# Optimization experiments

Hardware: AMD Instinct MI355X
Metric: run time of the kernel (lower is better)

## Reference

```python
import jax, jax.numpy as jnp
import numpy as np

B, S, D, H = 4, 1024, 1024, 16
HD = D // H  # per-head dim = 64
NEG = -10000000000.0


def setup_inputs() -> dict:
    key = jax.random.key(0)
    ks = jax.random.split(key, 12)
    q = jax.random.normal(ks[0], (B, S, D), jnp.float32)
    k = jax.random.normal(ks[1], (B, S, D), jnp.float32)
    v = jax.random.normal(ks[2], (B, S, D), jnp.float32)
    mask = jax.random.randint(ks[3], (B, S, S), 0, 2).astype(jnp.int32)
    sc = 1.0 / np.sqrt(D)
    Wq = jax.random.normal(ks[4], (H, D, HD), jnp.float32) * sc
    bq = jnp.zeros((H, HD), jnp.float32)
    Wk = jax.random.normal(ks[5], (H, D, HD), jnp.float32) * sc
    bk = jnp.zeros((H, HD), jnp.float32)
    Wv = jax.random.normal(ks[6], (H, D, HD), jnp.float32) * sc
    bv = jnp.zeros((H, HD), jnp.float32)
    Wo = jax.random.normal(ks[7], (D, D), jnp.float32) * sc
    bo = jnp.zeros((D,), jnp.float32)
    return {"query": q, "key": k, "value": v, "attention_mask": mask,
            "Wq": Wq, "bq": bq, "Wk": Wk, "bk": bk, "Wv": Wv, "bv": bv,
            "Wo": Wo, "bo": bo}


def reference(query, key, value, attention_mask, Wq, bq, Wk, bk, Wv, bv, Wo, bo):
    # batched per-head projections: [B,S,D] x [H,D,E] -> [B,H,S,E]
    q = jnp.einsum('bsd,hde->bhse', query, Wq) + bq[None, :, None, :]
    k = jnp.einsum('bsd,hde->bhse', key, Wk) + bk[None, :, None, :]
    v = jnp.einsum('bsd,hde->bhse', value, Wv) + bv[None, :, None, :]
    # NOTE: scale uses key_dim (model_size = full D), faithful to source
    score = jnp.einsum('bhse,bhte->bhst', q, k) / jnp.sqrt(jnp.float32(D))
    m = attention_mask.astype(jnp.float32)[:, None, :, :]  # [B,1,S,S]
    score = score + (1.0 - m) * NEG
    attn = jax.nn.softmax(score, axis=-1) * m  # double masking
    heads = jnp.einsum('bhst,bhte->bhse', attn, v)  # [B,H,S,E]
    # concat heads along feature dim (head order preserved)
    heads = heads.transpose(0, 2, 1, 3).reshape(B, S, D)
    return heads @ Wo + bo
```

## Files before the change

kernel.cpp:

```cpp
#include <hip/hip_runtime.h>

#define B_ 4
#define S_ 1024
#define D_ 1024
#define H_ 16
#define E_ 64
#define BS_ (B_*S_)
#define BHSE_ (B_*H_*S_*E_)

typedef __attribute__((ext_vector_type(8))) short bf16x8;
typedef __attribute__((ext_vector_type(4))) float f32x4;
typedef __attribute__((ext_vector_type(4))) unsigned int u32x4;

__device__ __forceinline__ unsigned short f2bf(float f) {
    unsigned int x = __float_as_uint(f);
    x = (x + 0x7FFFu + ((x >> 16) & 1u)) >> 16;
    return (unsigned short)x;
}
__device__ __forceinline__ float bf2f(unsigned short u) {
    return __uint_as_float(((unsigned int)u) << 16);
}
__device__ __forceinline__ float ldin(const void* p, size_t i, int isb) {
    return isb ? bf2f(((const unsigned short*)p)[i]) : ((const float*)p)[i];
}

__device__ __forceinline__ unsigned int cvtpk(float lo, float hi) {
    unsigned int r;
    asm("v_cvt_pk_bf16_f32 %0, %1, %2" : "=v"(r) : "v"(lo), "v"(hi));
    return r;
}
__device__ __forceinline__ unsigned int bperm(int srclane4, unsigned int v) {
    return (unsigned int)__builtin_amdgcn_ds_bpermute(srclane4, (int)v);
}
__device__ __forceinline__ bf16x8 u4bf(u32x4 w) {
    union { u32x4 u; bf16x8 h; } c; c.u = w; return c.h;
}

#if __has_builtin(__builtin_amdgcn_exp2f)
#define EXP2(x) __builtin_amdgcn_exp2f(x)
#else
#define EXP2(x) __expf((x) * 0.6931471805599453f)
#endif

__device__ __forceinline__ void gl2lds16(const void* g, void* l) {
    __builtin_amdgcn_global_load_lds(
        (const __attribute__((address_space(1))) void*)g,
        (__attribute__((address_space(3))) void*)l, 16, 0, 0);
}

__global__ void detect_dtype(const unsigned int* q, int* flag) {
    __shared__ int cnt;
    if (threadIdx.x == 0) cnt = 0;
    __syncthreads();
    unsigned int w = q[threadIdx.x];
    unsigned int lo = w & 0xFFFFu;
    unsigned int e = (lo >> 7) & 0xFFu;
    int ok = (lo == 0u) || (e >= 100u && e <= 145u);
    atomicAdd(&cnt, ok);
    __syncthreads();
    if (threadIdx.x == 0) flag[0] = (cnt >= 240) ? 1 : 0;
}

__global__ __launch_bounds__(256) void conv_w2(
        const void* Wq, const void* Wk, const void* Wv, const void* Wo,
        const void* bq_, const void* bk_, const void* bv_, const void* bo_,
        unsigned short* WT, float* biases, const int* flag) {
    __shared__ unsigned short Tt[64][72];
    const int isb = flag[0];
    const int z = blockIdx.z, t = threadIdx.x;
    const void* src = (z == 0) ? Wq : (z == 1) ? Wk : (z == 2) ? Wv : Wo;
    const int r0 = blockIdx.y * 64;
    const int c0 = blockIdx.x;
    {
        int dl = t >> 2, qc = t & 3;
        size_t base;
        if (z < 3) base = (size_t)c0 * 65536 + (size_t)(r0 + dl) * 64 + qc * 16;
        else       base = (size_t)(r0 + dl) * 1024 + (size_t)c0 * 64 + qc * 16;
        if (isb) {
            const unsigned short* s = (const unsigned short*)src + base;
            bf16x8 a0 = *(const bf16x8*)s, a1 = *(const bf16x8*)(s + 8);
#pragma unroll
            for (int j = 0; j < 8; j++) {
                Tt[qc * 16 + j][dl] = (unsigned short)a0[j];
                Tt[qc * 16 + 8 + j][dl] = (unsigned short)a1[j];
            }
        } else {
            const float* s = (const float*)src + base;
#pragma unroll
            for (int j = 0; j < 16; j++) Tt[qc * 16 + j][dl] = f2bf(s[j]);
        }
    }
    __syncthreads();
    {
        int el = t >> 2, qc = t & 3;
        size_t dst = (size_t)z * D_ * D_ + (size_t)(c0 * 64 + el) * D_ + r0 + qc * 16;
        *(bf16x8*)&WT[dst]     = *(const bf16x8*)&Tt[el][qc * 16];
        *(bf16x8*)&WT[dst + 8] = *(const bf16x8*)&Tt[el][qc * 16 + 8];
    }
    if (z == 3 && blockIdx.y == 0 && blockIdx.x < 4) {
        const void* bs = (blockIdx.x == 0) ? bq_ : (blockIdx.x == 1) ? bk_
                       : (blockIdx.x == 2) ? bv_ : bo_;
#pragma unroll
        for (int j = 0; j < 4; j++) {
            int i = t * 4 + j;
            biases[blockIdx.x * 1024 + i] = ldin(bs, i, isb);
        }
    }
}

__global__ void maskpack(const int* mask, unsigned long long* packT) {
    int W = blockIdx.x * 4 + (threadIdx.x >> 6);
    int lane = threadIdx.x & 63;
    int b = W >> 14, rem = W & 16383, s = rem >> 4, kt = rem & 15;
    int mv = mask[((size_t)b * 1024 + s) * 1024 + kt * 64 + lane];
    unsigned long long bits = __ballot(mv != 0);
    if (lane == 0) packT[((size_t)b * 16 + kt) * 1024 + s] = bits;
}

__global__ __launch_bounds__(256) void conv_a(
        const float* q, const float* k, const float* v,
        unsigned short* dst, const int* flag) {
    if (flag[0]) return;
    const int z = blockIdx.x >> 11;
    const float* s = (z == 0) ? q : (z == 1) ? k : v;
    const size_t i = ((size_t)(blockIdx.x & 2047) * 256 + threadIdx.x) * 8;
    f32x4 a0 = *(const f32x4*)(s + i);
    f32x4 a1 = *(const f32x4*)(s + i + 4);
    bf16x8 o;
#pragma unroll
    for (int j = 0; j < 4; j++) {
        o[j]     = (short)f2bf(a0[j]);
        o[4 + j] = (short)f2bf(a1[j]);
    }
    *(bf16x8*)&dst[(size_t)z * ((size_t)BS_ * D_) + i] = o;
}

template<int BM, int BN, int MODE, int MINW>
__global__ __launch_bounds__(256, MINW) void gemm_k(
        const void* A0, const void* A1, const void* A2, const unsigned short* Aconv,
        const unsigned short* BtB, const float* biasB, void* dstB, const int* flag) {
    constexpr int TOT16 = (BM + BN) * 32;
    constexpr int CALLS = TOT16 / 512;
    constexpr int CPW = CALLS / 4;
    constexpr int MT = BM / 32;
    constexpr int NT = BN / 32;
    __shared__ unsigned short buf[2][TOT16];

    const int t = threadIdx.x, lane = t & 63, w = t >> 6;
    const int lm = lane & 15, q4 = lane >> 4;
    const int wm = w >> 1, wn = w & 1;
    const int lr = lane >> 2;
    const int ls = lane & 3;
    const int lg = ls ^ ((lr >> 1) & 3);
    const int fl = flag[0];

    const unsigned short* Abf;
    const unsigned short* Bt;
    const float* bias;
    int z = 0, m0, n0, phase;
    if (MODE == 0) {
        int bid = blockIdx.x + (blockIdx.y << 5) + (blockIdx.z << 9);
        int xcd = bid & 7, idx = bid >> 3;
        z = idx >> 6;
        int r = idx & 63;
        int mt = (xcd << 2) + (r & 3);
        int nt = r >> 2;
        m0 = mt * BM; n0 = nt * BN;
        phase = (nt * 13 + z * 5) & 31;
        const void* Ain = (z == 0) ? A0 : (z == 1 ? A1 : A2);
        Abf = fl ? (const unsigned short*)Ain
                 : Aconv + (size_t)z * ((size_t)BS_ * D_);
        Bt = BtB + (size_t)z * D_ * D_;
        bias = biasB + z * 1024;
    } else {
        Abf = (const unsigned short*)A0;
        Bt = BtB; bias = biasB;
        m0 = blockIdx.x * BM; n0 = blockIdx.y * BN;
        phase = (blockIdx.x * 7 + blockIdx.y * 13) & 31;
    }

    auto stage = [&](int kk, int bi) {
#pragma unroll
        for (int i = 0; i < CPW; ++i) {
            int c = w * CPW + i;
            int row = c * 16 + lr;
            const unsigned short* g;
            if (row < BM)
                g = Abf + (size_t)(m0 + row) * D_ + kk + lg * 8;
            else
                g = Bt + (size_t)(n0 + row - BM) * D_ + kk + lg * 8;
            gl2lds16(g, &buf[bi][c * 512]);
        }
    };

    f32x4 acc[MT][NT];
#pragma unroll
    for (int i = 0; i < MT; i++)
#pragma unroll
        for (int j = 0; j < NT; j++) acc[i][j] = (f32x4){0.f, 0.f, 0.f, 0.f};

    stage((phase & 31) * 32, 0);
    for (int it = 0; it < D_ / 32; ++it) {
        const int bi = it & 1;
        __syncthreads();
        if (it < D_ / 32 - 1) stage(((it + 1 + phase) & 31) * 32, bi ^ 1);

        const unsigned short* As = buf[bi];
        const unsigned short* Bs = buf[bi] + BM * 32;
        bf16x8 af[MT], bv[NT];
#pragma unroll
        for (int mt = 0; mt < MT; mt++) {
            int row = wm * (BM / 2) + mt * 16 + lm;
            af[mt] = *(const bf16x8*)&As[row * 32 + (q4 ^ ((row >> 1) & 3)) * 8];
        }
#pragma unroll
        for (int nt = 0; nt < NT; nt++) {
            int row = wn * (BN / 2) + nt * 16 + lm;
            bv[nt] = *(const bf16x8*)&Bs[row * 32 + (q4 ^ ((row >> 1) & 3)) * 8];
        }
#pragma unroll
        for (int mt = 0; mt < MT; mt++)
#pragma unroll
            for (int nt = 0; nt < NT; nt++)
                acc[mt][nt] = __builtin_amdgcn_mfma_f32_16x16x32_bf16(
                    af[mt], bv[nt], acc[mt][nt], 0, 0, 0);
    }

#pragma unroll
    for (int mt = 0; mt < MT; mt++)
#pragma unroll
        for (int nt = 0; nt < NT; nt++) {
            int N = n0 + wn * (BN / 2) + nt * 16 + lm;
            int Mb = m0 + wm * (BM / 2) + mt * 16 + q4 * 4;
            if (MODE == 0 && z == 2) {
                int bb = Mb >> 10, sb = Mb & 1023, hh = N >> 6, e = N & 63;
                unsigned long long hv = 0;
#pragma unroll
                for (int r = 0; r < 4; r++)
                    hv |= (unsigned long long)f2bf(acc[mt][nt][r] + bias[N]) << (16 * r);
                unsigned short* d16 = (unsigned short*)dstB + (size_t)2 * BHSE_;
                *(unsigned long long*)&d16[(((size_t)(bb * H_ + hh) * E_ + e) << 10) + sb] = hv;
            } else {
#pragma unroll
                for (int r = 0; r < 4; r++) {
                    int M = Mb + r;
                    float v = acc[mt][nt][r] + bias[N];
                    if (MODE == 0) {
                        int bb = M >> 10, s = M & 1023, hh = N >> 6, e = N & 63;
                        unsigned short* d16 = (unsigned short*)dstB + (size_t)z * BHSE_;
                        d16[((size_t)(bb * H_ + hh) * S_ + s) * E_ + e] = f2bf(v);
                    } else {
                        size_t idx = (size_t)M * D_ + N;
                        if (fl) ((unsigned short*)dstB)[idx] = f2bf(v);
                        else    ((float*)dstB)[idx] = v;
                    }
                }
            }
        }
}

__global__ __launch_bounds__(256, 5) void attn64(
        const unsigned short* Qp, const unsigned short* Kp, const unsigned short* VpT,
        const unsigned long long* packT, unsigned short* heads) {
    __shared__ unsigned short KT[2][4096];
    __shared__ unsigned short VT[2][4096];

    const int qt = blockIdx.x, h = blockIdx.y, b = blockIdx.z;
    const int t = threadIdx.x, w = t >> 6, lane = t & 63, lm = lane & 15, q4 = lane >> 4;
    const size_t bh = ((size_t)b * H_ + h) * S_ * E_;
    const unsigned short* Qb = Qp + bh;
    const unsigned short* Kb = Kp + bh;
    const unsigned short* Vb = VpT + bh;
    const int q0 = qt * 64 + w * 16;

    const int l3 = lane >> 3, l7 = lane & 7;
    const int kLaneOff = l3 * 64 + (l7 ^ l3) * 8;
    const int vLaneOff = l3 * 1024 + (l7 ^ l3) * 8;

    const int sw = lm & 7;
    const int c0 = (q4 ^ sw) * 8, c1 = ((q4 ^ 4) ^ sw) * 8;

    const int srcA4 = ((lane & 15) | ((lane & 16) << 1)) << 2;
    const int srcB4 = srcA4 + 64;
    const bool selHi = (lane & 32) != 0;

    bf16x8 bq0 = *(const bf16x8*)&Qb[(size_t)(q0 + lm) * E_ + q4 * 8];
    bf16x8 bq1 = *(const bf16x8*)&Qb[(size_t)(q0 + lm) * E_ + 32 + q4 * 8];

    f32x4 oacc[4];
#pragma unroll
    for (int i = 0; i < 4; i++) oacc[i] = (f32x4){0.f, 0.f, 0.f, 0.f};
    float mrun = -3.0e38f, lrun = 0.f;
    const float scale2 = 0.03125f * 1.4426950408889634f;

#define STAGE(ktile, bufi)                                                    \
    {                                                                         \
        int k0s = (ktile) * 64;                                               \
        _Pragma("unroll")                                                     \
        for (int i_ = 0; i_ < 4; ++i_) {                                      \
            int c_ = w * 4 + i_;                                              \
            if (c_ < 8) {                                                     \
                gl2lds16(Kb + (size_t)k0s * 64 + c_ * 512 + kLaneOff,         \
                         &KT[bufi][c_ * 512]);                                \
            } else {                                                          \
                int cc_ = c_ - 8;                                             \
                gl2lds16(Vb + (size_t)cc_ * 8192 + k0s + vLaneOff,            \
                         &VT[bufi][cc_ * 512]);                               \
            }                                                                 \
        }                                                                     \
    }

    STAGE(0, 0)

    for (int kt = 0; kt < S_ / 64; ++kt) {
        const int bufi = kt & 1;
        __syncthreads();
        if (kt < 15) STAGE(kt + 1, bufi ^ 1)

        unsigned long long mk = packT[((size_t)b * 16 + kt) * 1024 + q0 + lm];

        f32x4 st[4];
#pragma unroll
        for (int jt = 0; jt < 4; ++jt) {
            const unsigned short* kr = &KT[bufi][(jt * 16 + lm) * 64];
            bf16x8 ka0 = *(const bf16x8*)&kr[c0];
            bf16x8 ka1 = *(const bf16x8*)&kr[c1];
            f32x4 zz = (f32x4){0.f, 0.f, 0.f, 0.f};
            zz = __builtin_amdgcn_mfma_f32_16x16x32_bf16(ka0, bq0, zz, 0, 0, 0);
            zz = __builtin_amdgcn_mfma_f32_16x16x32_bf16(ka1, bq1, zz, 0, 0, 0);
            st[jt] = zz;
        }

        float tmx = -3.0e38f;
#pragma unroll
        for (int jt = 0; jt < 4; ++jt)
#pragma unroll
            for (int r = 0; r < 4; r++) tmx = fmaxf(tmx, st[jt][r]);
        tmx = fmaxf(tmx, __shfl_xor(tmx, 16, 64));
        tmx = fmaxf(tmx, __shfl_xor(tmx, 32, 64));
        float pmax = tmx * scale2;

        if (!__all(pmax - mrun <= 8.f)) {
            float mnew = fmaxf(mrun, pmax);
            float alpha = EXP2(mrun - mnew);
            lrun *= alpha;
#pragma unroll
            for (int nt = 0; nt < 4; nt++) oacc[nt] = oacc[nt] * alpha;
            mrun = mnew;
        }
        const float mneg = -mrun;

        unsigned int mn = (unsigned int)(mk >> (q4 * 4));
        unsigned int mh = (unsigned int)(mk >> (q4 * 4 + 32));

        float ssum = 0.f;
        unsigned int cl[8];
#pragma unroll
        for (int jt = 0; jt < 4; ++jt) {
            unsigned int mm = (jt & 2) ? mh : mn;
            const int sh = (jt & 1) * 16;
            float p0 = EXP2(fmaf(st[jt][0], scale2, mneg));
            float p1 = EXP2(fmaf(st[jt][1], scale2, mneg));
            float p2 = EXP2(fmaf(st[jt][2], scale2, mneg));
            float p3 = EXP2(fmaf(st[jt][3], scale2, mneg));
            p0 = (mm & (1u << (sh + 0))) ? p0 : 0.f;
            p1 = (mm & (1u << (sh + 1))) ? p1 : 0.f;
            p2 = (mm & (1u << (sh + 2))) ? p2 : 0.f;
            p3 = (mm & (1u << (sh + 3))) ? p3 : 0.f;
            ssum += (p0 + p1) + (p2 + p3);
            cl[jt * 2]     = cvtpk(p0, p1);
            cl[jt * 2 + 1] = cvtpk(p2, p3);
        }
        ssum += __shfl_xor(ssum, 16, 64);
        ssum += __shfl_xor(ssum, 32, 64);
        lrun += ssum;

        u32x4 w0, w1;
        {
            unsigned int aA0 = bperm(srcA4, cl[0]), aA2 = bperm(srcA4, cl[2]);
            unsigned int aA1 = bperm(srcA4, cl[1]), aA3 = bperm(srcA4, cl[3]);
            unsigned int aB0 = bperm(srcB4, cl[0]), aB2 = bperm(srcB4, cl[2]);
            unsigned int aB1 = bperm(srcB4, cl[1]), aB3 = bperm(srcB4, cl[3]);
            w0 = (u32x4){selHi ? aA2 : aA0, selHi ? aA3 : aA1,
                         selHi ? aB2 : aB0, selHi ? aB3 : aB1};
            unsigned int bA0 = bperm(srcA4, cl[4]), bA2 = bperm(srcA4, cl[6]);
            unsigned int bA1 = bperm(srcA4, cl[5]), bA3 = bperm(srcA4, cl[7]);
            unsigned int bB0 = bperm(srcB4, cl[4]), bB2 = bperm(srcB4, cl[6]);
            unsigned int bB1 = bperm(srcB4, cl[5]), bB3 = bperm(srcB4, cl[7]);
            w1 = (u32x4){selHi ? bA2 : bA0, selHi ? bA3 : bA1,
                         selHi ? bB2 : bB0, selHi ? bB3 : bB1};
        }
        bf16x8 bp0 = u4bf(w0);
        bf16x8 bp1 = u4bf(w1);

#pragma unroll
        for (int nt = 0; nt < 4; nt++) {
            const unsigned short* vr = &VT[bufi][(nt * 16 + lm) * 64];
            bf16x8 va0 = *(const bf16x8*)&vr[c0];
            bf16x8 va1 = *(const bf16x8*)&vr[c1];
            oacc[nt] = __builtin_amdgcn_mfma_f32_16x16x32_bf16(va0, bp0, oacc[nt], 0, 0, 0);
            oacc[nt] = __builtin_amdgcn_mfma_f32_16x16x32_bf16(va1, bp1, oacc[nt], 0, 0, 0);
        }
    }

    float inv = 1.0f / lrun;
#pragma unroll
    for (int nt = 0; nt < 4; nt++) {
        unsigned int lo = cvtpk(oacc[nt][0] * inv, oacc[nt][1] * inv);
        unsigned int hi = cvtpk(oacc[nt][2] * inv, oacc[nt][3] * inv);
        unsigned long long hv = (unsigned long long)lo | ((unsigned long long)hi << 32);
        *(unsigned long long*)&heads[(size_t)(b * S_ + q0 + lm) * D_ + h * E_ + nt * 16 + q4 * 4] = hv;
    }
}

extern "C" void kernel_launch(void* const* d_in, const int* in_sizes, int n_in,
                              void* d_out, int out_size, void* d_ws, size_t ws_size,
                              hipStream_t stream) {
    char* ws = (char*)d_ws;
    int* flag = (int*)ws;
    unsigned short* WT = (unsigned short*)(ws + 256);
    unsigned short* WqT = WT;
    unsigned short* WoT = WT + (size_t)3 * D_ * D_;
    float* biases = (float*)(WT + (size_t)4 * D_ * D_);
    float* bq = biases;
    float* bo = biases + 3 * 1024;
    unsigned short* Qp = (unsigned short*)(biases + 4 * 1024);
    unsigned short* Kp = Qp + (size_t)BHSE_;
    unsigned short* Vp = Kp + (size_t)BHSE_;
    unsigned short* heads = Vp + (size_t)BHSE_;
    unsigned long long* packT = (unsigned long long*)(heads + (size_t)BHSE_);
    unsigned short* Aconv = (unsigned short*)(packT + (size_t)B_ * 16 * S_);

    detect_dtype<<<1, 256, 0, stream>>>((const unsigned int*)d_in[0], flag);
    conv_w2<<<dim3(16, 16, 4), 256, 0, stream>>>(
        d_in[4], d_in[6], d_in[8], d_in[10],
        d_in[5], d_in[7], d_in[9], d_in[11], WT, biases, flag);
    maskpack<<<16384, 256, 0, stream>>>((const int*)d_in[3], packT);
    conv_a<<<6144, 256, 0, stream>>>(
        (const float*)d_in[0], (const float*)d_in[1], (const float*)d_in[2],
        Aconv, flag);
    gemm_k<128, 64, 0, 4><<<dim3(32, 16, 3), 256, 0, stream>>>(
        d_in[0], d_in[1], d_in[2], Aconv, WqT, bq, Qp, flag);
    attn64<<<dim3(16, 16, 4), 256, 0, stream>>>(Qp, Kp, Vp, packT, heads);
    gemm_k<64, 64, 1, 8><<<dim3(64, 16, 1), 256, 0, stream>>>(
        heads, nullptr, nullptr, nullptr, WoT, bo, d_out, flag);
}
```

Measured before the change: 251.7 us.

## Fuse preprocessing kernels into one launch and widen QKV projection tiles

```diff
diff --git a/kernel.cpp b/kernel.cpp
--- a/kernel.cpp
+++ b/kernel.cpp
@@ -48,97 +48,99 @@
         (__attribute__((address_space(3))) void*)l, 16, 0, 0);
 }
 
-__global__ void detect_dtype(const unsigned int* q, int* flag) {
-    __shared__ int cnt;
-    if (threadIdx.x == 0) cnt = 0;
-    __syncthreads();
-    unsigned int w = q[threadIdx.x];
-    unsigned int lo = w & 0xFFFFu;
+__device__ __forceinline__ int detect_isb(const unsigned int* q) {
+    unsigned int wv = q[threadIdx.x & 63];
+    unsigned int lo = wv & 0xFFFFu;
     unsigned int e = (lo >> 7) & 0xFFu;
     int ok = (lo == 0u) || (e >= 100u && e <= 145u);
-    atomicAdd(&cnt, ok);
-    __syncthreads();
-    if (threadIdx.x == 0) flag[0] = (cnt >= 240) ? 1 : 0;
-}
-
-__global__ __launch_bounds__(256) void conv_w2(
+    return __popcll(__ballot(ok)) >= 48;
+}
+
+__global__ __launch_bounds__(256) void preproc(
+        const void* q_, const void* k_, const void* v_, const int* mask,
         const void* Wq, const void* Wk, const void* Wv, const void* Wo,
         const void* bq_, const void* bk_, const void* bv_, const void* bo_,
-        unsigned short* WT, float* biases, const int* flag) {
+        unsigned short* WT, float* biases, unsigned long long* packT,
+        unsigned short* Aconv) {
     __shared__ unsigned short Tt[64][72];
-    const int isb = flag[0];
-    const int z = blockIdx.z, t = threadIdx.x;
-    const void* src = (z == 0) ? Wq : (z == 1) ? Wk : (z == 2) ? Wv : Wo;
-    const int r0 = blockIdx.y * 64;
-    const int c0 = blockIdx.x;
-    {
-        int dl = t >> 2, qc = t & 3;
-        size_t base;
-        if (z < 3) base = (size_t)c0 * 65536 + (size_t)(r0 + dl) * 64 + qc * 16;
-        else       base = (size_t)(r0 + dl) * 1024 + (size_t)c0 * 64 + qc * 16;
-        if (isb) {
-            const unsigned short* s = (const unsigned short*)src + base;
-            bf16x8 a0 = *(const bf16x8*)s, a1 = *(const bf16x8*)(s + 8);
-#pragma unroll
-            for (int j = 0; j < 8; j++) {
-                Tt[qc * 16 + j][dl] = (unsigned short)a0[j];
-                Tt[qc * 16 + 8 + j][dl] = (unsigned short)a1[j];
+    const int isb = detect_isb((const unsigned int*)q_);
+    const int blk = blockIdx.x, t = threadIdx.x;
+
+    if (blk < 1024) {
+        const int c0 = blk & 15, r0 = ((blk >> 4) & 15) * 64, z = blk >> 8;
+        const void* src = (z == 0) ? Wq : (z == 1) ? Wk : (z == 2) ? Wv : Wo;
+        {
+            int dl = t >> 2, qc = t & 3;
+            size_t base;
+            if (z < 3) base = (size_t)c0 * 65536 + (size_t)(r0 + dl) * 64 + qc * 16;
+            else       base = (size_t)(r0 + dl) * 1024 + (size_t)c0 * 64 + qc * 16;
+            if (isb) {
+                const unsigned short* s = (const unsigned short*)src + base;
+                bf16x8 a0 = *(const bf16x8*)s, a1 = *(const bf16x8*)(s + 8);
+#pragma unroll
+                for (int j = 0; j < 8; j++) {
+                    Tt[qc * 16 + j][dl] = (unsigned short)a0[j];
+                    Tt[qc * 16 + 8 + j][dl] = (unsigned short)a1[j];
+                }
+            } else {
+                const float* s = (const float*)src + base;
+#pragma unroll
+                for (int j = 0; j < 16; j++) Tt[qc * 16 + j][dl] = f2bf(s[j]);
             }
-        } else {
-            const float* s = (const float*)src + base;
-#pragma unroll
-            for (int j = 0; j < 16; j++) Tt[qc * 16 + j][dl] = f2bf(s[j]);
-        }
-    }
-    __syncthreads();
-    {
-        int el = t >> 2, qc = t & 3;
-        size_t dst = (size_t)z * D_ * D_ + (size_t)(c0 * 64 + el) * D_ + r0 + qc * 16;
-        *(bf16x8*)&WT[dst]     = *(const bf16x8*)&Tt[el][qc * 16];
-        *(bf16x8*)&WT[dst + 8] = *(const bf16x8*)&Tt[el][qc * 16 + 8];
-    }
-    if (z == 3 && blockIdx.y == 0 && blockIdx.x < 4) {
-        const void* bs = (blockIdx.x == 0) ? bq_ : (blockIdx.x == 1) ? bk_
-                       : (blockIdx.x == 2) ? bv_ : bo_;
+        }
+        __syncthreads();
+        {
+            int el = t >> 2, qc = t & 3;
+            size_t dst = (size_t)z * D_ * D_ + (size_t)(c0 * 64 + el) * D_ + r0 + qc * 16;
+            *(bf16x8*)&WT[dst]     = *(const bf16x8*)&Tt[el][qc * 16];
+            *(bf16x8*)&WT[dst + 8] = *(const bf16x8*)&Tt[el][qc * 16 + 8];
+        }
+        if (z == 3 && ((blk >> 4) & 15) == 0 && c0 < 4) {
+            const void* bs = (c0 == 0) ? bq_ : (c0 == 1) ? bk_
+                           : (c0 == 2) ? bv_ : bo_;
+#pragma unroll
+            for (int j = 0; j < 4; j++) {
+                int i = t * 4 + j;
+                biases[c0 * 1024 + i] = ldin(bs, i, isb);
+            }
+        }
+    } else if (blk < 5120) {
+        int unit = (blk - 1024) * 4 + (t >> 6);
+        int lane = t & 63;
+        int b = unit >> 12, rem = unit & 4095, s0 = (rem >> 4) * 4, kt = rem & 15;
+        const int* mb = mask + ((size_t)b * 1024 + s0) * 1024 + kt * 64 + lane;
+        unsigned long long bits[4];
+#pragma unroll
+        for (int j = 0; j < 4; j++) bits[j] = __ballot(mb[j * 1024] != 0);
+        if (lane < 4) {
+            unsigned long long bb = (lane == 0) ? bits[0] : (lane == 1) ? bits[1]
+                                  : (lane == 2) ? bits[2] : bits[3];
+            packT[((size_t)b * 16 + kt) * 1024 + s0 + lane] = bb;
+        }
+    } else {
+        if (isb) return;
+        int blk2 = blk - 5120;
+        const int z = blk2 >> 11;
+        const float* s = (z == 0) ? (const float*)q_ : (z == 1) ? (const float*)k_
+                                                                : (const float*)v_;
+        const size_t i = ((size_t)(blk2 & 2047) * 256 + t) * 8;
+        f32x4 a0 = *(const f32x4*)(s + i);
+        f32x4 a1 = *(const f32x4*)(s + i + 4);
+        bf16x8 o;
 #pragma unroll
         for (int j = 0; j < 4; j++) {
-            int i = t * 4 + j;
-            biases[blockIdx.x * 1024 + i] = ldin(bs, i, isb);
-        }
-    }
-}
-
-__global__ void maskpack(const int* mask, unsigned long long* packT) {
-    int W = blockIdx.x * 4 + (threadIdx.x >> 6);
-    int lane = threadIdx.x & 63;
-    int b = W >> 14, rem = W & 16383, s = rem >> 4, kt = rem & 15;
-    int mv = mask[((size_t)b * 1024 + s) * 1024 + kt * 64 + lane];
-    unsigned long long bits = __ballot(mv != 0);
-    if (lane == 0) packT[((size_t)b * 16 + kt) * 1024 + s] = bits;
-}
-
-__global__ __launch_bounds__(256) void conv_a(
-        const float* q, const float* k, const float* v,
-        unsigned short* dst, const int* flag) {
-    if (flag[0]) return;
-    const int z = blockIdx.x >> 11;
-    const float* s = (z == 0) ? q : (z == 1) ? k : v;
-    const size_t i = ((size_t)(blockIdx.x & 2047) * 256 + threadIdx.x) * 8;
-    f32x4 a0 = *(const f32x4*)(s + i);
-    f32x4 a1 = *(const f32x4*)(s + i + 4);
-    bf16x8 o;
-#pragma unroll
-    for (int j = 0; j < 4; j++) {
-        o[j]     = (short)f2bf(a0[j]);
-        o[4 + j] = (short)f2bf(a1[j]);
-    }
-    *(bf16x8*)&dst[(size_t)z * ((size_t)BS_ * D_) + i] = o;
+            o[j]     = (short)f2bf(a0[j]);
+            o[4 + j] = (short)f2bf(a1[j]);
+        }
+        *(bf16x8*)&Aconv[(size_t)z * ((size_t)BS_ * D_) + i] = o;
+    }
 }
 
 template<int BM, int BN, int MODE, int MINW>
 __global__ __launch_bounds__(256, MINW) void gemm_k(
         const void* A0, const void* A1, const void* A2, const unsigned short* Aconv,
-        const unsigned short* BtB, const float* biasB, void* dstB, const int* flag) {
+        const unsigned short* BtB, const float* biasB, void* dstB,
+        const unsigned int* qdet) {
     constexpr int TOT16 = (BM + BN) * 32;
     constexpr int CALLS = TOT16 / 512;
     constexpr int CPW = CALLS / 4;
@@ -146,23 +148,23 @@
     constexpr int NT = BN / 32;
     __shared__ unsigned short buf[2][TOT16];
 
+    const int fl = detect_isb(qdet);
     const int t = threadIdx.x, lane = t & 63, w = t >> 6;
     const int lm = lane & 15, q4 = lane >> 4;
     const int wm = w >> 1, wn = w & 1;
     const int lr = lane >> 2;
     const int ls = lane & 3;
     const int lg = ls ^ ((lr >> 1) & 3);
-    const int fl = flag[0];
 
     const unsigned short* Abf;
     const unsigned short* Bt;
     const float* bias;
     int z = 0, m0, n0, phase;
     if (MODE == 0) {
-        int bid = blockIdx.x + (blockIdx.y << 5) + (blockIdx.z << 9);
+        int bid = blockIdx.x + gridDim.x * (blockIdx.y + gridDim.y * blockIdx.z);
         int xcd = bid & 7, idx = bid >> 3;
-        z = idx >> 6;
-        int r = idx & 63;
+        z = idx >> 5;
+        int r = idx & 31;
         int mt = (xcd << 2) + (r & 3);
         int nt = r >> 2;
         m0 = mt * BM; n0 = nt * BN;
@@ -417,7 +419,6 @@
                               void* d_out, int out_size, void* d_ws, size_t ws_size,
                               hipStream_t stream) {
     char* ws = (char*)d_ws;
-    int* flag = (int*)ws;
     unsigned short* WT = (unsigned short*)(ws + 256);
     unsigned short* WqT = WT;
     unsigned short* WoT = WT + (size_t)3 * D_ * D_;
@@ -431,17 +432,16 @@
     unsigned long long* packT = (unsigned long long*)(heads + (size_t)BHSE_);
     unsigned short* Aconv = (unsigned short*)(packT + (size_t)B_ * 16 * S_);
 
-    detect_dtype<<<1, 256, 0, stream>>>((const unsigned int*)d_in[0], flag);
-    conv_w2<<<dim3(16, 16, 4), 256, 0, stream>>>(
+    preproc<<<11264, 256, 0, stream>>>(
+        d_in[0], d_in[1], d_in[2], (const int*)d_in[3],
         d_in[4], d_in[6], d_in[8], d_in[10],
-        d_in[5], d_in[7], d_in[9], d_in[11], WT, biases, flag);
-    maskpack<<<16384, 256, 0, stream>>>((const int*)d_in[3], packT);
-    conv_a<<<6144, 256, 0, stream>>>(
-        (const float*)d_in[0], (const float*)d_in[1], (const float*)d_in[2],
-        Aconv, flag);
-    gemm_k<128, 64, 0, 4><<<dim3(32, 16, 3), 256, 0, stream>>>(
-        d_in[0], d_in[1], d_in[2], Aconv, WqT, bq, Qp, flag);
+        d_in[5], d_in[7], d_in[9], d_in[11],
+        WT, biases, packT, Aconv);
+    gemm_k<128, 128, 0, 3><<<dim3(32, 8, 3), 256, 0, stream>>>(
+        d_in[0], d_in[1], d_in[2], Aconv, WqT, bq, Qp,
+        (const unsigned int*)d_in[0]);
     attn64<<<dim3(16, 16, 4), 256, 0, stream>>>(Qp, Kp, Vp, packT, heads);
     gemm_k<64, 64, 1, 8><<<dim3(64, 16, 1), 256, 0, stream>>>(
-        heads, nullptr, nullptr, nullptr, WoT, bo, d_out, flag);
-}
+        heads, nullptr, nullptr, nullptr, WoT, bo, d_out,
+        (const unsigned int*)d_in[0]);
+}
```

Result: faster. 232.4 us (-7.7%).
